# Kernel optimization log

Hardware: AMD Instinct MI355X
Metric: run time of the kernel (lower is better)

## Reference

```python
import jax, jax.numpy as jnp
import numpy as np

PAD = 20  # (41 - 1) // 2, matches ReflectionPad2d(20)
CHANNELS = 6


def _matlab_gauss2d(shape=(41, 41), sigma=10.0):
    m, n = [(s - 1.0) / 2.0 for s in shape]
    y, x = np.ogrid[-m:m + 1, -n:n + 1]
    h = np.exp(-(x * x + y * y) / (2.0 * sigma * sigma))
    h[h < np.finfo(h.dtype).eps * h.max()] = 0
    s = h.sum()
    if s != 0:
        h /= s
    return h


def setup_inputs() -> dict:
    key = jax.random.key(0)
    x = jax.random.normal(key, (16, CHANNELS, 512, 512), dtype=jnp.float32)
    k = _matlab_gauss2d((41, 41), 10.0)  # [41, 41]
    # depthwise weight [C, 1, 41, 41], same kernel repeated per channel
    weight = jnp.asarray(np.repeat(k[None, None], CHANNELS, axis=0), dtype=jnp.float32)
    return {"x": x, "weight": weight}


def reference(x, weight):
    # reflect-pad H and W by 20 (PyTorch ReflectionPad2d semantics == jnp 'reflect')
    xp = jnp.pad(x, ((0, 0), (0, 0), (PAD, PAD), (PAD, PAD)), mode="reflect")
    # depthwise conv: feature_group_count = C, weight is [C, 1, kH, kW]
    out = jax.lax.conv_general_dilated(
        xp, weight,
        window_strides=(1, 1),
        padding="VALID",
        dimension_numbers=("NCHW", "OIHW", "NCHW"),
        feature_group_count=CHANNELS,
    )
    return out  # [B, C, H, W]
```

## Files before the change

kernel.cpp:

```cpp
#include <hip/hip_runtime.h>

#define KS 41
#define PAD 20
#define H 512
#define W 512
#define CH 6

#define TR 64
#define TC 64
#define PC (TC + 2 * PAD)
#define LSTR 65
#define WCOL 16
#define CWIN (WCOL + 2 * PAD)

__device__ __forceinline__ int reflect_idx(int i, int n) {
    if (i < 0) i = -i;
    if (i >= n) i = 2 * n - 2 - i;
    return i;
}

__device__ __forceinline__ int reflect511(int i) {
    return (H - 1) - abs((H - 1) - abs(i));
}

__device__ __forceinline__ float uniform_f(float v) {
    return __uint_as_float(__builtin_amdgcn_readfirstlane(__float_as_uint(v)));
}

__device__ __forceinline__ void load_coeffs(const float* __restrict__ w, int c,
                                            int lane, float gk[KS]) {
    float my = 0.f;
    if (lane < KS) {
        const float* wr = w + (size_t)c * KS * KS + (size_t)lane * KS;
        #pragma unroll
        for (int j = 0; j < KS; ++j) my += wr[j];
    }
    #pragma unroll
    for (int j = 0; j < KS; ++j)
        gk[j] = __uint_as_float(__builtin_amdgcn_readlane(__float_as_uint(my), j));
}

__global__ __launch_bounds__(256, 5)
void hblurT_kernel(const float* __restrict__ in, const float* __restrict__ w,
                   float* __restrict__ outT) {
    __shared__ float tmp[PC * LSTR];

    const int tid = threadIdx.x;
    const int wv  = tid >> 6;
    const int l   = tid & 63;
    const int img = blockIdx.z;
    const int c   = img % CH;
    const int c0  = blockIdx.x * TC;
    const int r0  = blockIdx.y * TR;

    float gk[KS];
    load_coeffs(w, c, l, gk);

    const float* ip = in + (size_t)img * H * W;
    #pragma unroll
    for (int k = 0; k < (TR * PC) / 256; ++k) {
        const int t = k * 256 + tid;
        const int r = t / PC;
        const int p = t - r * PC;
        tmp[p * LSTR + r] = ip[(size_t)(r0 + r) * W + reflect511(c0 - PAD + p)];
    }
    __syncthreads();

    float col[CWIN];
    #pragma unroll
    for (int i = 0; i < CWIN; ++i)
        col[i] = tmp[(WCOL * wv + i) * LSTR + l];

    float* op = outT + (size_t)img * H * W + (size_t)(c0 + WCOL * wv) * H + r0 + l;
    #pragma unroll
    for (int u = 0; u < WCOL; ++u) {
        float s = 0.f;
        #pragma unroll
        for (int j = 0; j < KS; ++j) s += gk[j] * col[u + j];
        op[(size_t)u * H] = s;
    }
}

#define TW 64
#define TH 128
#define TMPH (TH + 2 * PAD)

__global__ __launch_bounds__(256, 3)
void gauss_blur_fused_kernel(const float* __restrict__ x,
                             const float* __restrict__ w,
                             float* __restrict__ out) {
    __shared__ float g_s[KS];
    __shared__ float tmp[TMPH * TW];

    const int tid = threadIdx.x;
    const int bx = blockIdx.x, by = blockIdx.y, bz = blockIdx.z;
    const int c = bz % CH;

    if (tid < KS) {
        const float* wr = w + (size_t)c * KS * KS + (size_t)tid * KS;
        float s = 0.f;
        #pragma unroll
        for (int j = 0; j < KS; ++j) s += wr[j];
        g_s[tid] = s;
    }
    __syncthreads();

    float gr[KS];
    #pragma unroll
    for (int j = 0; j < KS; ++j) gr[j] = uniform_f(g_s[j]);

    const size_t img_off = (size_t)bz * (H * W);
    const float* img = x + img_off;
    const int x_tile = bx * TW;

    for (int gid = tid; gid < TMPH * (TW / 8); gid += 256) {
        const int r  = gid >> 3;
        const int gx = gid & 7;
        const int gy = reflect_idx(by * TH - PAD + r, H);
        const int x0 = x_tile + gx * 8;
        const float* row = img + (size_t)gy * W;

        float s[8];
        #pragma unroll
        for (int k = 0; k < 8; ++k) s[k] = 0.f;

        if (x0 >= PAD && x0 + 27 <= W - 1) {
            const float4* p = (const float4*)(row + x0 - PAD);
            #pragma unroll
            for (int m = 0; m < 12; ++m) {
                const float4 v = p[m];
                const float f[4] = {v.x, v.y, v.z, v.w};
                #pragma unroll
                for (int t = 0; t < 4; ++t) {
                    const int pos = 4 * m + t;
                    #pragma unroll
                    for (int k = 0; k < 8; ++k) {
                        const int tap = pos - k;
                        if (tap >= 0 && tap < KS) s[k] += gr[tap] * f[t];
                    }
                }
            }
        } else {
            #pragma unroll
            for (int pos = 0; pos < 48; ++pos) {
                const float f = row[reflect_idx(x0 - PAD + pos, W)];
                #pragma unroll
                for (int k = 0; k < 8; ++k) {
                    const int tap = pos - k;
                    if (tap >= 0 && tap < KS) s[k] += gr[tap] * f;
                }
            }
        }
        float* dstp = &tmp[r * TW + gx * 8];
        #pragma unroll
        for (int k = 0; k < 8; ++k) dstp[k] = s[k];
    }
    __syncthreads();

    const int lx = tid & 63;
    const int yg = tid >> 6;
    float* o = out + img_off;

    #pragma unroll
    for (int cc = 0; cc < 2; ++cc) {
        const int yc = yg * 32 + cc * 16;
        float col[56];
        #pragma unroll
        for (int i = 0; i < 56; ++i)
            col[i] = tmp[(yc + i) * TW + lx];
        #pragma unroll
        for (int y = 0; y < 16; ++y) {
            float s = 0.f;
            #pragma unroll
            for (int j = 0; j < KS; ++j) s += gr[j] * col[y + j];
            o[(size_t)(by * TH + yc + y) * W + x_tile + lx] = s;
        }
    }
}

extern "C" void kernel_launch(void* const* d_in, const int* in_sizes, int n_in,
                              void* d_out, int out_size, void* d_ws, size_t ws_size,
                              hipStream_t stream) {
    const float* x = (const float*)d_in[0];
    const float* w = (const float*)d_in[1];
    float* out = (float*)d_out;
    (void)in_sizes; (void)n_in; (void)out_size;

    const size_t need = (size_t)16 * CH * H * W * sizeof(float);
    if (ws_size >= need) {
        float* ws = (float*)d_ws;
        const dim3 grid(W / TC, H / TR, 16 * CH);
        hblurT_kernel<<<grid, 256, 0, stream>>>(x,  w, ws);
        hblurT_kernel<<<grid, 256, 0, stream>>>(ws, w, out);
    } else {
        dim3 grid(W / TW, H / TH, 16 * CH);
        gauss_blur_fused_kernel<<<grid, 256, 0, stream>>>(x, w, out);
    }
}
```

Before: 249.0 us.

## Precompute separable coefficients once and restructure tile load per column

Adds a tiny prep kernel that reduces each channel's 41x41 weight to row sums once, so the blur kernels read 41 precomputed coefficients instead of each block summing 41x41 weights. The tile load changes so that each thread owns one padded column, computes the reflection index once, and strides down rows. This removes per-element division and reflection math and keeps LDS writes contiguous. Launch bounds go from 5 to 6 blocks per SIMD. The cost is an extra kernel launch, and the global loads per wavefront now span columns within a row in a different pattern.

```diff
diff --git a/kernel.cpp b/kernel.cpp
--- a/kernel.cpp
+++ b/kernel.cpp
@@ -40,9 +40,23 @@
         gk[j] = __uint_as_float(__builtin_amdgcn_readlane(__float_as_uint(my), j));
 }
 
-__global__ __launch_bounds__(256, 5)
+__global__ void gauss_prep_kernel(const float* __restrict__ w,
+                                  float* __restrict__ cbuf) {
+    const int c = blockIdx.x;
+    const int j = threadIdx.x;
+    if (j < KS) {
+        const float* wr = w + (size_t)c * KS * KS + (size_t)j * KS;
+        float s = 0.f;
+        #pragma unroll
+        for (int k = 0; k < KS; ++k) s += wr[k];
+        cbuf[c * KS + j] = s;
+    }
+}
+
+template <bool GC>
+__global__ __launch_bounds__(256, 6)
 void hblurT_kernel(const float* __restrict__ in, const float* __restrict__ w,
-                   float* __restrict__ outT) {
+                   const float* __restrict__ gc, float* __restrict__ outT) {
     __shared__ float tmp[PC * LSTR];
 
     const int tid = threadIdx.x;
@@ -54,15 +68,25 @@
     const int r0  = blockIdx.y * TR;
 
     float gk[KS];
-    load_coeffs(w, c, l, gk);
-
-    const float* ip = in + (size_t)img * H * W;
-    #pragma unroll
-    for (int k = 0; k < (TR * PC) / 256; ++k) {
-        const int t = k * 256 + tid;
-        const int r = t / PC;
-        const int p = t - r * PC;
-        tmp[p * LSTR + r] = ip[(size_t)(r0 + r) * W + reflect511(c0 - PAD + p)];
+    if (GC) {
+        const float* g = gc + c * KS;
+        #pragma unroll
+        for (int j = 0; j < KS; ++j) gk[j] = uniform_f(g[j]);
+    } else {
+        load_coeffs(w, c, l, gk);
+    }
+
+    {
+        const int pcol = tid & 127;
+        const int rrow = tid >> 7;
+        if (pcol < PC) {
+            const int colr = reflect511(c0 - PAD + pcol);
+            const float* gp = in + (size_t)img * H * W + (size_t)(r0 + rrow) * W + colr;
+            float* lp = tmp + pcol * LSTR + rrow;
+            #pragma unroll
+            for (int k = 0; k < TR / 2; ++k)
+                lp[2 * k] = gp[(size_t)(2 * k) * W];
+        }
     }
     __syncthreads();
 
@@ -187,13 +211,20 @@
     (void)in_sizes; (void)n_in; (void)out_size;
 
     const size_t need = (size_t)16 * CH * H * W * sizeof(float);
-    if (ws_size >= need) {
+    const dim3 grid(W / TC, H / TR, 16 * CH);
+
+    if (ws_size >= need + 1024) {
         float* ws = (float*)d_ws;
-        const dim3 grid(W / TC, H / TR, 16 * CH);
-        hblurT_kernel<<<grid, 256, 0, stream>>>(x,  w, ws);
-        hblurT_kernel<<<grid, 256, 0, stream>>>(ws, w, out);
+        float* cbuf = ws + need / sizeof(float);
+        gauss_prep_kernel<<<dim3(CH), 64, 0, stream>>>(w, cbuf);
+        hblurT_kernel<true><<<grid, 256, 0, stream>>>(x,  w, cbuf, ws);
+        hblurT_kernel<true><<<grid, 256, 0, stream>>>(ws, w, cbuf, out);
+    } else if (ws_size >= need) {
+        float* ws = (float*)d_ws;
+        hblurT_kernel<false><<<grid, 256, 0, stream>>>(x,  w, nullptr, ws);
+        hblurT_kernel<false><<<grid, 256, 0, stream>>>(ws, w, nullptr, out);
     } else {
-        dim3 grid(W / TW, H / TH, 16 * CH);
-        gauss_blur_fused_kernel<<<grid, 256, 0, stream>>>(x, w, out);
-    }
-}
+        dim3 fgrid(W / TW, H / TH, 16 * CH);
+        gauss_blur_fused_kernel<<<fgrid, 256, 0, stream>>>(x, w, out);
+    }
+}
```

Result: faster. 234.4 us (-5.9%).
